# Optimization experiments

Measured on AMD Instinct MI355X. Metric: run time of the kernel, lower is better.

## Reference

```python
import jax, jax.numpy as jnp
import numpy as np

NUM_HEADS = 8
NUM_LEVELS = 4
NUM_POINTS = 4
EMBED_DIM = 256
HEAD_DIM = EMBED_DIM // NUM_HEADS  # 32
SUM_POINTS = NUM_LEVELS * NUM_POINTS  # 16
OFFSET_SCALE = 0.5
SPATIAL = [(80, 80), (40, 40), (20, 20), (10, 10)]


def _bilinear_gather(v_flat, x, y, H, W):
    """grid_sample(bilinear, padding zeros, align_corners=False) via gathers.
    v_flat: (BN, c, H*W); x, y: (BN, Lq, P) pixel coords. -> (BN, c, Lq*P)"""
    BN = v_flat.shape[0]
    x0 = jnp.floor(x)
    y0 = jnp.floor(y)
    wx1 = x - x0
    wy1 = y - y0

    def corner(xi, yi, w):
        valid = (xi >= 0) & (xi <= W - 1) & (yi >= 0) & (yi <= H - 1)
        xc = jnp.clip(xi, 0, W - 1).astype(jnp.int32)
        yc = jnp.clip(yi, 0, H - 1).astype(jnp.int32)
        idx = (yc * W + xc).reshape(BN, -1)  # (BN, Lq*P)
        g = jnp.take_along_axis(v_flat, idx[:, None, :], axis=2)  # (BN, c, Lq*P)
        return g * (w * valid).reshape(BN, 1, -1)

    return (corner(x0, y0, (1.0 - wx1) * (1.0 - wy1))
            + corner(x0 + 1.0, y0, wx1 * (1.0 - wy1))
            + corner(x0, y0 + 1.0, (1.0 - wx1) * wy1)
            + corner(x0 + 1.0, y0 + 1.0, wx1 * wy1))


def setup_inputs() -> dict:
    key = jax.random.key(0)
    ks = jax.random.split(key, 6)
    bs, Lq = 16, 300
    spatial = np.array(SPATIAL, dtype=np.int64)
    Lv = int((spatial[:, 0] * spatial[:, 1]).sum())  # 8500

    query = jax.random.normal(ks[0], (bs, Lq, EMBED_DIM), jnp.float32)
    reference_points = jax.random.uniform(ks[1], (bs, Lq, 1, 4), jnp.float32)  # cx,cy,w,h in (0,1)
    value = jax.random.normal(ks[2], (bs, NUM_HEADS, HEAD_DIM, Lv), jnp.float32)

    W_off = jax.random.normal(ks[3], (EMBED_DIM, NUM_HEADS * SUM_POINTS * 2), jnp.float32) * 0.01
    # bias from _reset_parameters grid init
    thetas = np.arange(NUM_HEADS, dtype=np.float32) * (2.0 * np.pi / NUM_HEADS)
    grid = np.stack([np.cos(thetas), np.sin(thetas)], -1)
    grid = grid / np.abs(grid).max(-1, keepdims=True)
    grid = np.tile(grid.reshape(NUM_HEADS, 1, 2), (1, SUM_POINTS, 1))
    scaling = np.concatenate([np.arange(1, NUM_POINTS + 1) for _ in range(NUM_LEVELS)]).reshape(1, -1, 1)
    b_off = jnp.asarray((grid * scaling).reshape(-1), jnp.float32)

    W_attn = jax.random.normal(ks[4], (EMBED_DIM, NUM_HEADS * SUM_POINTS), jnp.float32) * 0.01
    b_attn = jnp.zeros((NUM_HEADS * SUM_POINTS,), jnp.float32)
    num_points_scale = jnp.full((SUM_POINTS,), 1.0 / NUM_POINTS, jnp.float32)

    return {"query": query, "reference_points": reference_points, "value": value,
            "value_spatial_shapes": spatial, "W_off": W_off, "b_off": b_off,
            "W_attn": W_attn, "b_attn": b_attn, "num_points_scale": num_points_scale}


def reference(query, reference_points, value, value_spatial_shapes,
              W_off, b_off, W_attn, b_attn, num_points_scale):
    bs, Lq, _ = query.shape
    BN = bs * NUM_HEADS

    off = (query @ W_off + b_off).reshape(bs, Lq, NUM_HEADS, SUM_POINTS, 2)
    attn = jax.nn.softmax((query @ W_attn + b_attn).reshape(bs, Lq, NUM_HEADS, SUM_POINTS), axis=-1)

    # box branch: reference_points (bs, Lq, 1, 4); [..., 2:] = wh scales offsets
    offset = off * num_points_scale[:, None] * reference_points[:, :, None, :, 2:] * OFFSET_SCALE
    loc = reference_points[:, :, None, :, :2] + offset  # (bs, Lq, H, SUM_POINTS, 2) in [0,1]

    grids = 2.0 * loc - 1.0
    grids = jnp.transpose(grids, (0, 2, 1, 3, 4)).reshape(BN, Lq, SUM_POINTS, 2)
    attn = jnp.transpose(attn, (0, 2, 1, 3)).reshape(BN, 1, Lq, SUM_POINTS)

    shapes = np.asarray(value_spatial_shapes)
    lvl_sizes = (shapes[:, 0] * shapes[:, 1]).tolist()
    v_levels = jnp.split(value.reshape(BN, HEAD_DIM, -1), np.cumsum(lvl_sizes)[:-1], axis=2)
    g_levels = jnp.split(grids, np.arange(NUM_POINTS, SUM_POINTS, NUM_POINTS), axis=2)

    sampled = []
    for (H, W), v_l, g_l in zip(shapes.tolist(), v_levels, g_levels):
        # align_corners=False pixel coords
        x = (g_l[..., 0] + 1.0) * (W * 0.5) - 0.5
        y = (g_l[..., 1] + 1.0) * (H * 0.5) - 0.5
        s = _bilinear_gather(v_l, x, y, H, W).reshape(BN, HEAD_DIM, Lq, NUM_POINTS)
        sampled.append(s)
    sampled = jnp.concatenate(sampled, axis=-1)  # (BN, c, Lq, SUM_POINTS)

    out = (sampled * attn).sum(-1)  # (BN, c, Lq)
    out = out.reshape(bs, NUM_HEADS * HEAD_DIM, Lq).transpose(0, 2, 1)  # (bs, Lq, embed_dim)
    return out
```

## Files before the change

### kernel.cpp

```cpp
#include <hip/hip_runtime.h>
#include <hip/hip_bf16.h>
#include <hip/hip_fp16.h>
#include <math.h>

#define BS 16
#define LQ 300
#define NH 8
#define HD 32
#define SP 16
#define ED 256
#define LV 8500
#define NB_BLK 300
#define PXT 256
#define TR_PER_BN 34
#define NTR_BLK (TR_PER_BN * 128)
#define TSTR 264

static __device__ __forceinline__ int imin(int a, int b) { return a < b ? a : b; }
static __device__ __forceinline__ int imax(int a, int b) { return a > b ? a : b; }

static __device__ __forceinline__ unsigned f2bf(float x) {
    unsigned u = __float_as_uint(x);
    return (u + 0x7fffu + ((u >> 16) & 1u)) >> 16;
}

static __device__ __forceinline__ unsigned pk2h(float a, float b) {
    __half ha = __float2half_rn(a), hb = __float2half_rn(b);
    unsigned short ua = *reinterpret_cast<unsigned short*>(&ha);
    unsigned short ub = *reinterpret_cast<unsigned short*>(&hb);
    return (unsigned)ua | ((unsigned)ub << 16);
}

static __device__ __forceinline__ float2 up2h(unsigned u) {
    unsigned short ua = (unsigned short)(u & 0xffffu);
    unsigned short ub = (unsigned short)(u >> 16);
    __half ha = *reinterpret_cast<__half*>(&ua);
    __half hb = *reinterpret_cast<__half*>(&ub);
    return make_float2(__half2float(ha), __half2float(hb));
}

__global__ __launch_bounds__(256) void kF(const float* __restrict__ query,
                                          const float* __restrict__ refp,
                                          const float* __restrict__ Woff,
                                          const float* __restrict__ boff,
                                          const float* __restrict__ Wattn,
                                          const float* __restrict__ battn,
                                          const float* __restrict__ nps,
                                          unsigned* __restrict__ la,
                                          const float* __restrict__ v,
                                          __hip_bfloat16* __restrict__ vt,
                                          int nb) {
    __shared__ float s[32 * TSTR];
    const int tid = threadIdx.x;

    if ((int)blockIdx.x >= nb) {
        const int t   = blockIdx.x - nb;
        const int bn  = t / TR_PER_BN;
        const int px0 = (t - bn * TR_PER_BN) * PXT;
        const int nlv = imin(PXT, LV - px0);

        const int w   = tid >> 6;
        const int px4 = (tid & 63) * 4;
        const float* src = v + (size_t)bn * (HD * LV) + px0 + px4;
        float4 r[8];
        if (px4 < nlv) {
#pragma unroll
            for (int k = 0; k < 8; ++k) {
                int row = w + 4 * k;
                r[k] = *reinterpret_cast<const float4*>(src + (size_t)row * LV);
            }
#pragma unroll
            for (int k = 0; k < 8; ++k) {
                int row = w + 4 * k;
                *reinterpret_cast<float4*>(s + row * TSTR + px4) = r[k];
            }
        }
        __syncthreads();
        const int p2 = tid >> 2;
        const int q  = tid & 3;
        char* dst0 = (char*)vt + ((size_t)bn * LV + px0) * (HD * 2) + q * 16;
#pragma unroll
        for (int j = 0; j < 4; ++j) {
            int p = p2 + 64 * j;
            if (p < nlv) {
                unsigned pk[4];
#pragma unroll
                for (int i = 0; i < 4; ++i) {
                    float f0 = s[(8 * q + 2 * i) * TSTR + p];
                    float f1 = s[(8 * q + 2 * i + 1) * TSTR + p];
                    pk[i] = f2bf(f0) | (f2bf(f1) << 16);
                }
                *reinterpret_cast<uint4*>(dst0 + (size_t)p * 64) =
                    make_uint4(pk[0], pk[1], pk[2], pk[3]);
            }
        }
        return;
    }

    float* qbuf = s;
    float* lbuf = s;
    const int gq0 = blockIdx.x * 16;

    const float* qsrc = query + (size_t)gq0 * ED;
#pragma unroll
    for (int i = 0; i < 16; ++i) qbuf[tid + 256 * i] = qsrc[tid + 256 * i];
    __syncthreads();

    const int qi = tid >> 5;
    const int cl = tid & 31;
    const float* qa = qbuf + qi * ED;
    const float* qb = qbuf + (qi + 8) * ED;

    float a0[4] = {0,0,0,0}, a1[4] = {0,0,0,0}, a2[4] = {0,0,0,0};
    float c0[4] = {0,0,0,0}, c1[4] = {0,0,0,0}, c2[4] = {0,0,0,0};
    const float4* w0 = (const float4*)(Woff + cl * 4);
    const float4* w1 = (const float4*)(Woff + 128 + cl * 4);
    const float4* w2 = (const float4*)(Wattn + cl * 4);
#pragma unroll 4
    for (int k = 0; k < ED; ++k) {
        float va = qa[k], vb = qb[k];
        float4 x0 = w0[k * 64];
        float4 x1 = w1[k * 64];
        float4 x2 = w2[k * 32];
        a0[0] += va * x0.x; a0[1] += va * x0.y; a0[2] += va * x0.z; a0[3] += va * x0.w;
        a1[0] += va * x1.x; a1[1] += va * x1.y; a1[2] += va * x1.z; a1[3] += va * x1.w;
        a2[0] += va * x2.x; a2[1] += va * x2.y; a2[2] += va * x2.z; a2[3] += va * x2.w;
        c0[0] += vb * x0.x; c0[1] += vb * x0.y; c0[2] += vb * x0.z; c0[3] += vb * x0.w;
        c1[0] += vb * x1.x; c1[1] += vb * x1.y; c1[2] += vb * x1.z; c1[3] += vb * x1.w;
        c2[0] += vb * x2.x; c2[1] += vb * x2.y; c2[2] += vb * x2.z; c2[3] += vb * x2.w;
    }
    __syncthreads();
    {
        float* ra = lbuf + qi * 384;
        float* rb = lbuf + (qi + 8) * 384;
#pragma unroll
        for (int u = 0; u < 4; ++u) {
            float bo0 = boff[cl * 4 + u];
            float bo1 = boff[128 + cl * 4 + u];
            float ba  = battn[cl * 4 + u];
            ra[cl * 4 + u]       = a0[u] + bo0;
            ra[128 + cl * 4 + u] = a1[u] + bo1;
            ra[256 + cl * 4 + u] = a2[u] + ba;
            rb[cl * 4 + u]       = c0[u] + bo0;
            rb[128 + cl * 4 + u] = c1[u] + bo1;
            rb[256 + cl * 4 + u] = c2[u] + ba;
        }
    }
    __syncthreads();

#pragma unroll
    for (int it = 0; it < 2; ++it) {
        const int slot = it * 256 + tid;
        const int qi2 = slot >> 5;
        const int h2  = (slot >> 2) & 7;
        const int pg  = slot & 3;
        const float* lr = lbuf + qi2 * 384;

        float l[4];
#pragma unroll
        for (int i = 0; i < 4; ++i) l[i] = lr[256 + h2 * 16 + pg * 4 + i];
        float m = fmaxf(fmaxf(l[0], l[1]), fmaxf(l[2], l[3]));
        m = fmaxf(m, __shfl_xor(m, 1));
        m = fmaxf(m, __shfl_xor(m, 2));
        float e[4];
        float ps = 0.f;
#pragma unroll
        for (int i = 0; i < 4; ++i) { e[i] = expf(l[i] - m); ps += e[i]; }
        ps += __shfl_xor(ps, 1);
        ps += __shfl_xor(ps, 2);
        float inv = 1.f / ps;

        const int gq = gq0 + qi2;
        const int b  = gq / LQ;
        const int q  = gq - b * LQ;
        const float* rp = refp + (size_t)gq * 4;
        float cx = rp[0], cy = rp[1], rw = rp[2], rh = rp[3];

        const int Wl = 80 >> pg;
        const int base = (25600 - (25600 >> (2 * pg))) / 3;
        const float fw = (float)Wl;

        unsigned* dst = la + ((((size_t)b * NH + h2) * LQ + q) * SP + pg * 4) * 4;
#pragma unroll
        for (int i = 0; i < 4; ++i) {
            int p = pg * 4 + i;
            float ox = lr[h2 * 32 + p * 2 + 0];
            float oy = lr[h2 * 32 + p * 2 + 1];
            float sc = nps[p] * 0.5f;
            float locx = cx + ox * sc * rw;
            float locy = cy + oy * sc * rh;
            float x = locx * fw - 0.5f;
            float y = locy * fw - 0.5f;
            float aw = e[i] * inv;

            float x0f = floorf(x), y0f = floorf(y);
            float fx = x - x0f, fy = y - y0f;
            int ix0 = (int)x0f, iy0 = (int)y0f;
            int ix1 = ix0 + 1, iy1 = iy0 + 1;
            bool vx0 = (ix0 >= 0) && (ix0 < Wl);
            bool vx1 = (ix1 >= 0) && (ix1 < Wl);
            bool vy0 = (iy0 >= 0) && (iy0 < Wl);
            bool vy1 = (iy1 >= 0) && (iy1 < Wl);
            int cx0 = imin(imax(ix0, 0), Wl - 1);
            int cx1 = imin(imax(ix1, 0), Wl - 1);
            int cy0 = imin(imax(iy0, 0), Wl - 1);
            int cy1 = imin(imax(iy1, 0), Wl - 1);
            float w00 = aw * (1.f - fx) * (1.f - fy) * ((vx0 && vy0) ? 1.f : 0.f);
            float w10 = aw * fx * (1.f - fy) * ((vx1 && vy0) ? 1.f : 0.f);
            float w01 = aw * (1.f - fx) * fy * ((vx0 && vy1) ? 1.f : 0.f);
            float w11 = aw * fx * fy * ((vx1 && vy1) ? 1.f : 0.f);
            unsigned i00 = (unsigned)(base + cy0 * Wl + cx0);
            unsigned i10 = (unsigned)(base + cy0 * Wl + cx1);
            unsigned i01 = (unsigned)(base + cy1 * Wl + cx0);
            unsigned i11 = (unsigned)(base + cy1 * Wl + cx1);

            *reinterpret_cast<uint4*>(dst + i * 4) =
                make_uint4(pk2h(w00, w10), pk2h(w01, w11),
                           i00 | (i10 << 16), i01 | (i11 << 16));
        }
    }
}

__global__ __launch_bounds__(128) void kC4(const __hip_bfloat16* __restrict__ vt,
                                           const unsigned* __restrict__ la,
                                           float* __restrict__ out) {
    const int bid = blockIdx.x;
    const int logical = (bid & 7) * 160 + (bid >> 3);
    const int bh = logical / 10;
    const int qt = logical - bh * 10;
    const int b = bh >> 3;
    const int h = bh & 7;

    const int tid = threadIdx.x;
    const int qs = tid >> 2;
    const int l4 = tid & 3;
    const int q = qt * 32 + qs;
    if (q >= LQ) return;

    const unsigned* lq = la + (((size_t)bh * LQ + q) * SP) * 4;
    const char* vb = (const char*)vt + (size_t)bh * LV * (HD * 2) + l4 * 16;

    float acc[8] = {0.f, 0.f, 0.f, 0.f, 0.f, 0.f, 0.f, 0.f};

#pragma unroll 2
    for (int p = 0; p < SP; p += 2) {
        uint4 rec0 = *reinterpret_cast<const uint4*>(lq + p * 4);
        uint4 rec1 = *reinterpret_cast<const uint4*>(lq + p * 4 + 4);
        uint4 r0 = *reinterpret_cast<const uint4*>(vb + (size_t)(rec0.z & 0xffffu) * 64);
        uint4 r1 = *reinterpret_cast<const uint4*>(vb + (size_t)(rec0.z >> 16) * 64);
        uint4 r2 = *reinterpret_cast<const uint4*>(vb + (size_t)(rec0.w & 0xffffu) * 64);
        uint4 r3 = *reinterpret_cast<const uint4*>(vb + (size_t)(rec0.w >> 16) * 64);
        uint4 r4 = *reinterpret_cast<const uint4*>(vb + (size_t)(rec1.z & 0xffffu) * 64);
        uint4 r5 = *reinterpret_cast<const uint4*>(vb + (size_t)(rec1.z >> 16) * 64);
        uint4 r6 = *reinterpret_cast<const uint4*>(vb + (size_t)(rec1.w & 0xffffu) * 64);
        uint4 r7 = *reinterpret_cast<const uint4*>(vb + (size_t)(rec1.w >> 16) * 64);
        float2 wA0 = up2h(rec0.x), wB0 = up2h(rec0.y);
        float2 wA1 = up2h(rec1.x), wB1 = up2h(rec1.y);
#define FMA8(W, R)                                                             \
        {                                                                      \
            union { unsigned u; float f; } _t;                                 \
            _t.u = (R).x << 16;         acc[0] = fmaf((W), _t.f, acc[0]);      \
            _t.u = (R).x & 0xffff0000u; acc[1] = fmaf((W), _t.f, acc[1]);      \
            _t.u = (R).y << 16;         acc[2] = fmaf((W), _t.f, acc[2]);      \
            _t.u = (R).y & 0xffff0000u; acc[3] = fmaf((W), _t.f, acc[3]);      \
            _t.u = (R).z << 16;         acc[4] = fmaf((W), _t.f, acc[4]);      \
            _t.u = (R).z & 0xffff0000u; acc[5] = fmaf((W), _t.f, acc[5]);      \
            _t.u = (R).w << 16;         acc[6] = fmaf((W), _t.f, acc[6]);      \
            _t.u = (R).w & 0xffff0000u; acc[7] = fmaf((W), _t.f, acc[7]);      \
        }
        FMA8(wA0.x, r0) FMA8(wA0.y, r1) FMA8(wB0.x, r2) FMA8(wB0.y, r3)
        FMA8(wA1.x, r4) FMA8(wA1.y, r5) FMA8(wB1.x, r6) FMA8(wB1.y, r7)
#undef FMA8
    }
    float* op = out + ((size_t)b * LQ + q) * ED + h * HD + l4 * 8;
    *reinterpret_cast<float4*>(op)     = make_float4(acc[0], acc[1], acc[2], acc[3]);
    *reinterpret_cast<float4*>(op + 4) = make_float4(acc[4], acc[5], acc[6], acc[7]);
}

__global__ __launch_bounds__(320) void kCfb(const float* __restrict__ val,
                                            const unsigned* __restrict__ la,
                                            float* __restrict__ out) {
    __shared__ __align__(16) unsigned sla[10 * SP * 4];
    int bid = blockIdx.x;
    int logical = (bid & 7) * 480 + (bid >> 3);
    int bh = logical / 30;
    int qt = logical - bh * 30;
    int b = bh >> 3;
    int h = bh & 7;
    const int tid = threadIdx.x;
    const unsigned* lsrc = la + (((size_t)bh * LQ + qt * 10) * SP) * 4;
    for (int i = tid; i < 640; i += 320) sla[i] = lsrc[i];
    __syncthreads();
    const int qs = tid >> 5;
    const int c  = tid & 31;
    const float* vb = val + ((size_t)bh * HD + c) * LV;
    float acc = 0.f;
    const unsigned* lq = sla + qs * (SP * 4);
#pragma unroll
    for (int p = 0; p < SP; ++p) {
        uint4 rec = *reinterpret_cast<const uint4*>(lq + p * 4);
        float2 wA = up2h(rec.x), wB = up2h(rec.y);
        acc += wA.x * vb[rec.z & 0xffffu];
        acc += wA.y * vb[rec.z >> 16];
        acc += wB.x * vb[rec.w & 0xffffu];
        acc += wB.y * vb[rec.w >> 16];
    }
    int q = qt * 10 + qs;
    out[((size_t)b * LQ + q) * ED + h * HD + c] = acc;
}

extern "C" void kernel_launch(void* const* d_in, const int* in_sizes, int n_in,
                              void* d_out, int out_size, void* d_ws, size_t ws_size,
                              hipStream_t stream) {
    const float* query = (const float*)d_in[0];
    const float* refp  = (const float*)d_in[1];
    const float* value = (const float*)d_in[2];
    const float* Woff  = (const float*)d_in[4];
    const float* boff  = (const float*)d_in[5];
    const float* Wattn = (const float*)d_in[6];
    const float* battn = (const float*)d_in[7];
    const float* nps   = (const float*)d_in[8];
    float* out = (float*)d_out;

    const size_t la_bytes = (size_t)BS * NH * LQ * SP * 16;
    const size_t vt_bytes = (size_t)BS * NH * LV * HD * sizeof(__hip_bfloat16);
    unsigned* la = (unsigned*)d_ws;
    __hip_bfloat16* vt = (__hip_bfloat16*)((char*)d_ws + la_bytes);
    const bool use_tr = ws_size >= la_bytes + vt_bytes;

    if (use_tr) {
        kF<<<dim3(NB_BLK + NTR_BLK), 256, 0, stream>>>(query, refp, Woff, boff,
                                                       Wattn, battn, nps, la,
                                                       value, vt, NB_BLK);
        kC4<<<dim3(1280), 128, 0, stream>>>(vt, la, out);
    } else {
        kF<<<dim3(NB_BLK), 256, 0, stream>>>(query, refp, Woff, boff,
                                             Wattn, battn, nps, la,
                                             value, (__hip_bfloat16*)nullptr, NB_BLK);
        kCfb<<<dim3(3840), 320, 0, stream>>>(value, la, out);
    }
}
```

Baseline: 73.27 us.

## Process four transpose tiles per block with register prefetch of next tile

The value transpose/bf16 conversion blocks now each handle four consecutive 256-pixel tiles instead of one, cutting the number of transpose blocks by four. While one tile is converted from shared memory and written out, the global loads for the next tile are issued into registers, overlapping load latency with the store phase. This adds an extra barrier per tile and reduces block-level parallelism for the transpose stage. The launch grid size depends on NTR_BLK, which is now redefined accordingly.

```diff
diff --git a/kernel.cpp b/kernel.cpp
--- a/kernel.cpp
+++ b/kernel.cpp
@@ -13,7 +13,9 @@
 #define NB_BLK 300
 #define PXT 256
 #define TR_PER_BN 34
-#define NTR_BLK (TR_PER_BN * 128)
+#define NTILES (TR_PER_BN * 128)
+#define TPB 4
+#define NTR_BLK (NTILES / TPB)
 #define TSTR 264
 
 static __device__ __forceinline__ int imin(int a, int b) { return a < b ? a : b; }
@@ -54,45 +56,66 @@
     const int tid = threadIdx.x;
 
     if ((int)blockIdx.x >= nb) {
-        const int t   = blockIdx.x - nb;
-        const int bn  = t / TR_PER_BN;
-        const int px0 = (t - bn * TR_PER_BN) * PXT;
-        const int nlv = imin(PXT, LV - px0);
-
+        const int blk = blockIdx.x - nb;
         const int w   = tid >> 6;
         const int px4 = (tid & 63) * 4;
-        const float* src = v + (size_t)bn * (HD * LV) + px0 + px4;
+        const int p2  = tid >> 2;
+        const int q   = tid & 3;
+        const int t0  = blk * TPB;
+
+        int bn  = t0 / TR_PER_BN;
+        int ti  = t0 - bn * TR_PER_BN;
+        int px0 = ti * PXT;
+        int nlv = imin(PXT, LV - px0);
         float4 r[8];
         if (px4 < nlv) {
-#pragma unroll
-            for (int k = 0; k < 8; ++k) {
-                int row = w + 4 * k;
-                r[k] = *reinterpret_cast<const float4*>(src + (size_t)row * LV);
+            const float* src = v + (size_t)bn * (HD * LV) + px0 + px4;
+#pragma unroll
+            for (int k = 0; k < 8; ++k)
+                r[k] = *reinterpret_cast<const float4*>(src + (size_t)(w + 4 * k) * LV);
+        }
+
+#pragma unroll
+        for (int tt = 0; tt < TPB; ++tt) {
+            if (px4 < nlv) {
+#pragma unroll
+                for (int k = 0; k < 8; ++k)
+                    *reinterpret_cast<float4*>(s + (w + 4 * k) * TSTR + px4) = r[k];
             }
-#pragma unroll
-            for (int k = 0; k < 8; ++k) {
-                int row = w + 4 * k;
-                *reinterpret_cast<float4*>(s + row * TSTR + px4) = r[k];
+            __syncthreads();
+            const int cbn = bn, cpx0 = px0, cnlv = nlv;
+
+            if (tt + 1 < TPB) {
+                const int t1 = t0 + tt + 1;
+                bn  = t1 / TR_PER_BN;
+                ti  = t1 - bn * TR_PER_BN;
+                px0 = ti * PXT;
+                nlv = imin(PXT, LV - px0);
+                if (px4 < nlv) {
+                    const float* src = v + (size_t)bn * (HD * LV) + px0 + px4;
+#pragma unroll
+                    for (int k = 0; k < 8; ++k)
+                        r[k] = *reinterpret_cast<const float4*>(src + (size_t)(w + 4 * k) * LV);
+                }
             }
-        }
-        __syncthreads();
-        const int p2 = tid >> 2;
-        const int q  = tid & 3;
-        char* dst0 = (char*)vt + ((size_t)bn * LV + px0) * (HD * 2) + q * 16;
-#pragma unroll
-        for (int j = 0; j < 4; ++j) {
-            int p = p2 + 64 * j;
-            if (p < nlv) {
-                unsigned pk[4];
-#pragma unroll
-                for (int i = 0; i < 4; ++i) {
-                    float f0 = s[(8 * q + 2 * i) * TSTR + p];
-                    float f1 = s[(8 * q + 2 * i + 1) * TSTR + p];
-                    pk[i] = f2bf(f0) | (f2bf(f1) << 16);
+
+            char* dst0 = (char*)vt + ((size_t)cbn * LV + cpx0) * (HD * 2) + q * 16;
+#pragma unroll
+            for (int j = 0; j < 4; ++j) {
+                int p = p2 + 64 * j;
+                if (p < cnlv) {
+                    unsigned pk[4];
+#pragma unroll
+                    for (int i = 0; i < 4; ++i) {
+                        float f0 = s[(8 * q + 2 * i) * TSTR + p];
+                        float f1 = s[(8 * q + 2 * i + 1) * TSTR + p];
+                        pk[i] = f2bf(f0) | (f2bf(f1) << 16);
+                    }
+                    *reinterpret_cast<uint4*>(dst0 + (size_t)p * 64) =
+                        make_uint4(pk[0], pk[1], pk[2], pk[3]);
                 }
-                *reinterpret_cast<uint4*>(dst0 + (size_t)p * 64) =
-                    make_uint4(pk[0], pk[1], pk[2], pk[3]);
             }
+            __syncthreads();
         }
         return;
     }
```

Result: slower. 121.5 us (+65.8%).
